# Kernel optimization log

Measured on AMD Instinct MI355X. Metric: run time of the kernel, lower is better.

Reference implementation:

```python
import jax, jax.numpy as jnp
import numpy as np

STRIDE = 8
RATIOS = (0.33, 0.5, 1.0, 2.0, 3.0)
SCALES = (8,)
SEARCH = 255
SCORE = 25                      # (255-127)//8 + 1 + 8
A = len(RATIOS) * len(SCALES)   # 5 anchors per location
THR_HIGH = 0.6
THR_LOW = 0.3
POS_NUM = 16
TOTAL_NUM = 64


def _gen_anchors():
    # Replicates pysot Anchors.generate_all_anchors (corner format, flattened y,x,a)
    base = np.zeros((A, 4), dtype=np.float32)
    sz = STRIDE * STRIDE
    c = 0
    for r in RATIOS:
        ws = int(np.sqrt(sz / r)); hs = int(ws * r)
        for s in SCALES:
            w = ws * s; h = hs * s
            base[c] = [-w * 0.5, -h * 0.5, w * 0.5, h * 0.5]
            c += 1
    ori = SEARCH // 2 - (SCORE // 2) * STRIDE
    xs = ori + STRIDE * np.arange(SCORE, dtype=np.float32)
    cx, cy = np.meshgrid(xs, xs)  # row index = y, col index = x
    ctr = np.stack([cx, cy, cx, cy], -1).reshape(SCORE, SCORE, 1, 4)
    return (base.reshape(1, 1, A, 4) + ctr).reshape(-1, 4).astype(np.float32)


def setup_inputs() -> dict:
    key = jax.random.key(0)
    b, G = 128, 64
    k1, k2 = jax.random.split(key)
    xy = jax.random.uniform(k1, (b, G, 2), minval=0.0, maxval=170.0)
    wh = jax.random.uniform(k2, (b, G, 2), minval=20.0, maxval=70.0)
    gt_boxes = jnp.concatenate([xy, xy + wh], axis=-1)  # valid corner boxes in-image
    return {"gt_boxes": gt_boxes, "anchors": jnp.asarray(_gen_anchors()), "size": SCORE, "neg": 0}


def _overlaps(anchors, gt):
    aw = anchors[:, 2] - anchors[:, 0] + 1.0
    ah = anchors[:, 3] - anchors[:, 1] + 1.0
    area_a = (aw * ah)[None, :, None]
    gw = gt[..., 2] - gt[..., 0] + 1.0
    gh = gt[..., 3] - gt[..., 1] + 1.0
    area_g = (gw * gh)[:, None, :]
    ix = (jnp.minimum(anchors[None, :, None, 2], gt[:, None, :, 2])
          - jnp.maximum(anchors[None, :, None, 0], gt[:, None, :, 0]) + 1.0)
    iy = (jnp.minimum(anchors[None, :, None, 3], gt[:, None, :, 3])
          - jnp.maximum(anchors[None, :, None, 1], gt[:, None, :, 1]) + 1.0)
    inter = jnp.clip(ix, 0.0) * jnp.clip(iy, 0.0)
    return inter / (area_a + area_g - inter)


def _transform(anchors, gt):
    # anchors (N,4), gt (b,N,4) -> (b,N,4) deltas (dx,dy,dw,dh)
    aw = anchors[:, 2] - anchors[:, 0] + 1.0
    ah = anchors[:, 3] - anchors[:, 1] + 1.0
    acx = anchors[:, 0] + 0.5 * aw
    acy = anchors[:, 1] + 0.5 * ah
    gw = gt[..., 2] - gt[..., 0] + 1.0
    gh = gt[..., 3] - gt[..., 1] + 1.0
    gcx = gt[..., 0] + 0.5 * gw
    gcy = gt[..., 1] + 0.5 * gh
    dx = (gcx - acx[None]) / aw[None]
    dy = (gcy - acy[None]) / ah[None]
    dw = jnp.log(gw / aw[None])
    dh = jnp.log(gh / ah[None])
    return jnp.stack([dx, dy, dw, dh], axis=-1)


def reference(gt_boxes, anchors, size, neg):
    b = gt_boxes.shape[0]
    N = anchors.shape[0]
    ov = _overlaps(anchors, gt_boxes)          # (b,N,G) dominant intermediate
    max_ov = jnp.max(ov, axis=2)               # (b,N)
    arg = jnp.argmax(ov, axis=2)               # (b,N)
    gt_max = jnp.max(ov, axis=1)               # (b,G)

    cls = jnp.full((b, N), -1, dtype=jnp.int32)
    cls = jnp.where(max_ov >= THR_HIGH, 1, cls)
    cls = jnp.where(max_ov <= THR_LOW, 0, cls)
    gt_max = jnp.where(gt_max == 0.0, 1e-5, gt_max)
    keep = jnp.sum((ov == gt_max[:, None, :]).astype(jnp.int32), axis=2)
    cls = jnp.where(keep > 0, 1, cls)

    # Deterministic pos/neg subsampling (original uses np.random permutation;
    # we keep the first POS_NUM / TOTAL_NUM by anchor index per batch).
    pos = cls == 1
    cls = jnp.where(pos & (jnp.cumsum(pos.astype(jnp.int32), axis=1) > POS_NUM), -1, cls)
    negm = cls == 0
    cls = jnp.where(negm & (jnp.cumsum(negm.astype(jnp.int32), axis=1) > TOTAL_NUM), -1, cls)

    matched = jnp.take_along_axis(gt_boxes, arg[..., None], axis=1)  # (b,N,4)
    bt = _transform(anchors, matched)                                # (b,N,4)

    # Replicates original bug: pos_num taken from LAST batch element only.
    pos_num = jnp.sum((cls[-1] == 1).astype(jnp.int32))
    bw = jnp.where(cls == 1, 1.0 / pos_num.astype(gt_boxes.dtype), 0.0).astype(gt_boxes.dtype)

    # allowed_border is large -> all anchors inside -> _unmap is identity.
    cls_o = cls.reshape(b, size, size, A).transpose(0, 3, 1, 2)
    bt_o = bt.reshape(b, size, size, A, 4).transpose(0, 4, 3, 1, 2)
    bw_o = bw.reshape(b, size, size, A).transpose(0, 3, 1, 2)
    return cls_o, bt_o, bw_o, max_ov
```

## Files before the change

kernel.cpp:

```cpp
#include <hip/hip_runtime.h>


namespace {
constexpr int B_   = 128;
constexpr int N_   = 3125;
constexpr int G_   = 64;
constexpr int A_   = 5;
constexpr int S_   = 25;
constexpr int POSN = 16;
constexpr int TOTN = 64;

constexpr int CLS_OFF = 0;
constexpr int BT_OFF  = B_ * A_ * S_ * S_;
constexpr int BW_OFF  = BT_OFF + B_ * 4 * A_ * S_ * S_;
constexpr int MO_OFF  = BW_OFF + B_ * A_ * S_ * S_;
}

__device__ __forceinline__ float area_f(float x0, float y0, float x1, float y1) {
#pragma clang fp contract(off)
  return ((x1 - x0) + 1.0f) * ((y1 - y0) + 1.0f);
}

__device__ __forceinline__ float iou_f(float a0, float a1, float a2, float a3,
                                       float aarea, float g0, float g1,
                                       float g2, float g3, float garea) {
#pragma clang fp contract(off)
  float ix = (fminf(a2, g2) - fmaxf(a0, g0)) + 1.0f;
  float iy = (fminf(a3, g3) - fmaxf(a1, g1)) + 1.0f;
  ix = fmaxf(ix, 0.0f);
  iy = fmaxf(iy, 0.0f);
  float inter = ix * iy;
  return inter / ((aarea + garea) - inter);
}

__global__ __launch_bounds__(256) void k1_gtmax(
    const float* __restrict__ gt,
    const float* __restrict__ anchors,
    float* __restrict__ gtmax,
    int* __restrict__ poscnt) {
#pragma clang fp contract(off)
  if (blockIdx.x == 0 && threadIdx.x == 0) poscnt[0] = 0;

  const int t    = threadIdx.x;
  const int lane = t & 63;
  const int w    = blockIdx.x * 4 + (t >> 6);
  const int p0   = w * 2;
  const int b    = p0 >> 6;
  const int g0   = p0 & 63;

  const float4 gg0 = ((const float4*)gt)[b * G_ + g0];
  const float4 gg1 = ((const float4*)gt)[b * G_ + g0 + 1];
  const float ga0 = area_f(gg0.x, gg0.y, gg0.z, gg0.w);
  const float ga1 = area_f(gg1.x, gg1.y, gg1.z, gg1.w);

  float m0 = 0.0f, m1 = 0.0f;
#pragma unroll 4
  for (int i = 0; i < 48; ++i) {
    const int n = i * 64 + lane;
    const float4 aa = ((const float4*)anchors)[n];
    const float aarea = area_f(aa.x, aa.y, aa.z, aa.w);
    m0 = fmaxf(m0, iou_f(aa.x, aa.y, aa.z, aa.w, aarea,
                         gg0.x, gg0.y, gg0.z, gg0.w, ga0));
    m1 = fmaxf(m1, iou_f(aa.x, aa.y, aa.z, aa.w, aarea,
                         gg1.x, gg1.y, gg1.z, gg1.w, ga1));
  }
  {
    const int n = 48 * 64 + lane;
    if (n < N_) {
      const float4 aa = ((const float4*)anchors)[n];
      const float aarea = area_f(aa.x, aa.y, aa.z, aa.w);
      m0 = fmaxf(m0, iou_f(aa.x, aa.y, aa.z, aa.w, aarea,
                           gg0.x, gg0.y, gg0.z, gg0.w, ga0));
      m1 = fmaxf(m1, iou_f(aa.x, aa.y, aa.z, aa.w, aarea,
                           gg1.x, gg1.y, gg1.z, gg1.w, ga1));
    }
  }
#pragma unroll
  for (int off = 32; off > 0; off >>= 1) {
    m0 = fmaxf(m0, __shfl_xor(m0, off, 64));
    m1 = fmaxf(m1, __shfl_xor(m1, off, 64));
  }
  if (lane == 0) {
    gtmax[p0]     = m0;
    gtmax[p0 + 1] = m1;
  }
}

__global__ __launch_bounds__(256) void k2_anchor(
    const float* __restrict__ gt, const float* __restrict__ anchors,
    const float* __restrict__ gtmax, float* __restrict__ out,
    int* __restrict__ cls0, int* __restrict__ poscnt) {
#pragma clang fp contract(off)
  const int b = blockIdx.y;
  const int t = threadIdx.x;
  const int n = blockIdx.x * 256 + t;

  __shared__ float s_gt[G_ * 4];
  __shared__ float s_garea[G_];
  __shared__ float s_gtmax[G_];
  __shared__ int   s_pc;

  if (t == 0) s_pc = 0;
  s_gt[t] = gt[b * G_ * 4 + t];
  __syncthreads();
  if (t < G_) {
    s_garea[t] =
        area_f(s_gt[t * 4 + 0], s_gt[t * 4 + 1], s_gt[t * 4 + 2], s_gt[t * 4 + 3]);
    const float v = gtmax[b * G_ + t];
    s_gtmax[t] = (v == 0.0f) ? 1e-5f : v;
  }
  __syncthreads();

  if (n < N_) {
    const float4 aa = ((const float4*)anchors)[n];
    const float aw = (aa.z - aa.x) + 1.0f;
    const float ah = (aa.w - aa.y) + 1.0f;
    const float aarea = aw * ah;

    float best = -1.0f;
    int barg = 0;
    int keep = 0;
#pragma unroll 8
    for (int g = 0; g < G_; ++g) {
      const float4 gg = *(const float4*)&s_gt[g * 4];
      const float v = iou_f(aa.x, aa.y, aa.z, aa.w, aarea,
                            gg.x, gg.y, gg.z, gg.w, s_garea[g]);
      if (v > best) { best = v; barg = g; }
      keep |= (v == s_gtmax[g]);
    }

    int cc = -1;
    if (best >= 0.6f) cc = 1;
    if (best <= 0.3f) cc = 0;
    if (keep) cc = 1;
    cls0[b * N_ + n] = cc;
    if (b == B_ - 1 && cc == 1) atomicAdd(&s_pc, 1);

    const float m0 = s_gt[barg * 4 + 0], m1 = s_gt[barg * 4 + 1];
    const float m2 = s_gt[barg * 4 + 2], m3 = s_gt[barg * 4 + 3];
    const float gw = (m2 - m0) + 1.0f;
    const float gh = (m3 - m1) + 1.0f;
    const float acx = aa.x + 0.5f * aw;
    const float acy = aa.y + 0.5f * ah;
    const float gcx = m0 + 0.5f * gw;
    const float gcy = m1 + 0.5f * gh;
    const float dx = (gcx - acx) / aw;
    const float dy = (gcy - acy) / ah;
    const float dw = logf(gw / aw);
    const float dh = logf(gh / ah);

    const int a = n % A_;
    const int rem = n / A_;
    const int x = rem % S_;
    const int y = rem / S_;
    const int spat = y * S_ + x;

    float* __restrict__ out_bt = out + BT_OFF;
    const int btb = ((b * 4 + 0) * A_ + a) * (S_ * S_) + spat;
    out_bt[btb + 0 * A_ * S_ * S_] = dx;
    out_bt[btb + 1 * A_ * S_ * S_] = dy;
    out_bt[btb + 2 * A_ * S_ * S_] = dw;
    out_bt[btb + 3 * A_ * S_ * S_] = dh;

    out[MO_OFF + b * N_ + n] = best;
  }
  __syncthreads();
  if (t == 0 && b == B_ - 1 && s_pc > 0) atomicAdd(poscnt, s_pc);
}

__global__ __launch_bounds__(256) void k3_caps_bw(
    float* __restrict__ out, const int* __restrict__ cls0,
    const int* __restrict__ poscnt) {
  const int b = blockIdx.x;
  const int t = threadIdx.x;
  __shared__ int s_c[N_];
  __shared__ int s_p[256];
  __shared__ int s_n[256];

#pragma unroll
  for (int k = 0; k < 13; ++k) {
    const int i = k * 256 + t;
    if (i < N_) s_c[i] = cls0[b * N_ + i];
  }
  __syncthreads();

  const int n0 = t * 13;
  int cvals[13];
  int myp = 0, myn = 0;
#pragma unroll
  for (int k = 0; k < 13; ++k) {
    const int n = n0 + k;
    int cc = -1;
    if (n < N_) {
      cc = s_c[n];
      if (cc == 1) ++myp;
      else if (cc == 0) ++myn;
    }
    cvals[k] = cc;
  }
  s_p[t] = myp;
  s_n[t] = myn;
  __syncthreads();
  for (int off = 1; off < 256; off <<= 1) {
    int vp = 0, vn = 0;
    if (t >= off) { vp = s_p[t - off]; vn = s_n[t - off]; }
    __syncthreads();
    s_p[t] += vp;
    s_n[t] += vn;
    __syncthreads();
  }

  int runp = s_p[t] - myp;
  int runn = s_n[t] - myn;
#pragma unroll
  for (int k = 0; k < 13; ++k) {
    const int n = n0 + k;
    if (n >= N_) break;
    int cc = cvals[k];
    if (cc == 1) {
      if (++runp > POSN) cc = -1;
    } else if (cc == 0) {
      if (++runn > TOTN) cc = -1;
    }
    s_c[n] = __float_as_int((float)cc);
  }
  __syncthreads();

  const int pc = poscnt[0];
  const float inv = 1.0f / (float)((pc < POSN) ? pc : POSN);

#pragma unroll
  for (int k = 0; k < 13; ++k) {
    const int o = k * 256 + t;
    if (o < N_) {
      const int a  = o / 625;
      const int sp = o % 625;
      const float v = __int_as_float(s_c[sp * 5 + a]);
      out[CLS_OFF + b * N_ + o] = v;
      out[BW_OFF + b * N_ + o] = (v == 1.0f) ? inv : 0.0f;
    }
  }
}

extern "C" void kernel_launch(void* const* d_in, const int* in_sizes, int n_in,
                              void* d_out, int out_size, void* d_ws,
                              size_t ws_size, hipStream_t stream) {
  const float* gt = (const float*)d_in[0];
  const float* anchors = (const float*)d_in[1];
  float* out = (float*)d_out;
  int* poscnt = (int*)d_ws;
  float* gtmax = (float*)d_ws + 64;
  int* cls0 = (int*)d_ws + 64 + B_ * G_;

  k1_gtmax<<<1024, 256, 0, stream>>>(gt, anchors, gtmax, poscnt);
  k2_anchor<<<dim3(13, B_), 256, 0, stream>>>(gt, anchors, gtmax, out, cls0,
                                              poscnt);
  k3_caps_bw<<<B_, 256, 0, stream>>>(out, cls0, poscnt);
}
```

Before: 113.7 us.

## Separable gt-max IoU via per-axis overlap and fuse cap kernel into anchor kernel

The gt-max kernel no longer scans all 3125 anchors. It uses the regular anchor grid: for each anchor shape it takes the maximum x-overlap and y-overlap across grid positions with wave shuffles and multiplies them, with anchor sizes and areas hard-coded as constants. The third kernel is folded into the second using a per-batch ticket counter, so the last block of each batch does the pos/neg capping. Blocks then spin until the last batch finishes before writing box weights. This removes one launch and most of the gt-max arithmetic, but it depends on the fixed anchor geometry and adds a cross-block spin wait that could stall or deadlock if blocks are not co-resident.

```diff
diff --git a/kernel.cpp b/kernel.cpp
--- a/kernel.cpp
+++ b/kernel.cpp
@@ -35,61 +35,53 @@
 
 __global__ __launch_bounds__(256) void k1_gtmax(
     const float* __restrict__ gt,
-    const float* __restrict__ anchors,
     float* __restrict__ gtmax,
-    int* __restrict__ poscnt) {
-#pragma clang fp contract(off)
-  if (blockIdx.x == 0 && threadIdx.x == 0) poscnt[0] = 0;
-
-  const int t    = threadIdx.x;
+    int* __restrict__ arr) {
+#pragma clang fp contract(off)
+  const int t = threadIdx.x;
+  if (blockIdx.x == 0 && t < 1 + B_) arr[t] = 0;
+
   const int lane = t & 63;
-  const int w    = blockIdx.x * 4 + (t >> 6);
-  const int p0   = w * 2;
-  const int b    = p0 >> 6;
-  const int g0   = p0 & 63;
-
-  const float4 gg0 = ((const float4*)gt)[b * G_ + g0];
-  const float4 gg1 = ((const float4*)gt)[b * G_ + g0 + 1];
-  const float ga0 = area_f(gg0.x, gg0.y, gg0.z, gg0.w);
-  const float ga1 = area_f(gg1.x, gg1.y, gg1.z, gg1.w);
-
-  float m0 = 0.0f, m1 = 0.0f;
-#pragma unroll 4
-  for (int i = 0; i < 48; ++i) {
-    const int n = i * 64 + lane;
-    const float4 aa = ((const float4*)anchors)[n];
-    const float aarea = area_f(aa.x, aa.y, aa.z, aa.w);
-    m0 = fmaxf(m0, iou_f(aa.x, aa.y, aa.z, aa.w, aarea,
-                         gg0.x, gg0.y, gg0.z, gg0.w, ga0));
-    m1 = fmaxf(m1, iou_f(aa.x, aa.y, aa.z, aa.w, aarea,
-                         gg1.x, gg1.y, gg1.z, gg1.w, ga1));
-  }
-  {
-    const int n = 48 * 64 + lane;
-    if (n < N_) {
-      const float4 aa = ((const float4*)anchors)[n];
-      const float aarea = area_f(aa.x, aa.y, aa.z, aa.w);
-      m0 = fmaxf(m0, iou_f(aa.x, aa.y, aa.z, aa.w, aarea,
-                           gg0.x, gg0.y, gg0.z, gg0.w, ga0));
-      m1 = fmaxf(m1, iou_f(aa.x, aa.y, aa.z, aa.w, aarea,
-                           gg1.x, gg1.y, gg1.z, gg1.w, ga1));
-    }
-  }
-#pragma unroll
-  for (int off = 32; off > 0; off >>= 1) {
-    m0 = fmaxf(m0, __shfl_xor(m0, off, 64));
-    m1 = fmaxf(m1, __shfl_xor(m1, off, 64));
-  }
-  if (lane == 0) {
-    gtmax[p0]     = m0;
-    gtmax[p0 + 1] = m1;
-  }
-}
-
-__global__ __launch_bounds__(256) void k2_anchor(
+  const int pair = blockIdx.x * 4 + (t >> 6);
+  const int b = pair >> 6;
+  const int g = pair & 63;
+
+  const float4 gg = ((const float4*)gt)[b * G_ + g];
+  const float garea = area_f(gg.x, gg.y, gg.z, gg.w);
+
+  const int half = lane >> 5;
+  const int p = lane & 31;
+  const float c = 31.0f + 8.0f * (float)p;
+  const float Glo = half ? gg.y : gg.x;
+  const float Ghi = half ? gg.w : gg.z;
+  const bool valid = p < S_;
+
+  const float HW[A_] = {52.f, 44.f, 32.f, 20.f, 16.f};
+  const float HH[A_] = {16.f, 20.f, 32.f, 40.f, 48.f};
+  const float AA[A_] = {3465.f, 3649.f, 4225.f, 3321.f, 3201.f};
+
+  float m = 0.0f;
+#pragma unroll
+  for (int s = 0; s < A_; ++s) {
+    const float H = half ? HH[s] : HW[s];
+    float v = (fminf(c + H, Ghi) - fmaxf(c - H, Glo)) + 1.0f;
+    v = fmaxf(v, 0.0f);
+    if (!valid) v = 0.0f;
+#pragma unroll
+    for (int off = 1; off < 32; off <<= 1)
+      v = fmaxf(v, __shfl_xor(v, off, 64));
+    const float other = __shfl_xor(v, 32, 64);
+    const float inter = v * other;
+    const float uni = (AA[s] + garea) - inter;
+    m = fmaxf(m, inter / uni);
+  }
+  if (lane == 0) gtmax[pair] = m;
+}
+
+__global__ __launch_bounds__(256) void k2_fused(
     const float* __restrict__ gt, const float* __restrict__ anchors,
     const float* __restrict__ gtmax, float* __restrict__ out,
-    int* __restrict__ cls0, int* __restrict__ poscnt) {
+    int* __restrict__ cls0, int* __restrict__ arr) {
 #pragma clang fp contract(off)
   const int b = blockIdx.y;
   const int t = threadIdx.x;
@@ -99,6 +91,11 @@
   __shared__ float s_garea[G_];
   __shared__ float s_gtmax[G_];
   __shared__ int   s_pc;
+  __shared__ int   s_ticket;
+  __shared__ float s_inv;
+  __shared__ int   s_c[N_];
+  __shared__ int   s_p[256];
+  __shared__ int   s_n[256];
 
   if (t == 0) s_pc = 0;
   s_gt[t] = gt[b * G_ * 4 + t];
@@ -133,7 +130,8 @@
     if (best >= 0.6f) cc = 1;
     if (best <= 0.3f) cc = 0;
     if (keep) cc = 1;
-    cls0[b * N_ + n] = cc;
+    __hip_atomic_store(&cls0[b * N_ + n], cc, __ATOMIC_RELAXED,
+                       __HIP_MEMORY_SCOPE_AGENT);
     if (b == B_ - 1 && cc == 1) atomicAdd(&s_pc, 1);
 
     const float m0 = s_gt[barg * 4 + 0], m1 = s_gt[barg * 4 + 1];
@@ -165,38 +163,35 @@
     out[MO_OFF + b * N_ + n] = best;
   }
   __syncthreads();
-  if (t == 0 && b == B_ - 1 && s_pc > 0) atomicAdd(poscnt, s_pc);
-}
-
-__global__ __launch_bounds__(256) void k3_caps_bw(
-    float* __restrict__ out, const int* __restrict__ cls0,
-    const int* __restrict__ poscnt) {
-  const int b = blockIdx.x;
-  const int t = threadIdx.x;
-  __shared__ int s_c[N_];
-  __shared__ int s_p[256];
-  __shared__ int s_n[256];
-
+
+  if (t == 0) {
+    if (b == B_ - 1 && s_pc > 0) atomicAdd(&arr[0], s_pc);
+    __threadfence();
+    s_ticket = atomicAdd(&arr[1 + b], 1);
+  }
+  __syncthreads();
+  if (s_ticket != 12) return;
+
+  __threadfence();
 #pragma unroll
   for (int k = 0; k < 13; ++k) {
     const int i = k * 256 + t;
-    if (i < N_) s_c[i] = cls0[b * N_ + i];
+    if (i < N_)
+      s_c[i] = __hip_atomic_load(&cls0[b * N_ + i], __ATOMIC_RELAXED,
+                                 __HIP_MEMORY_SCOPE_AGENT);
   }
   __syncthreads();
 
   const int n0 = t * 13;
-  int cvals[13];
   int myp = 0, myn = 0;
 #pragma unroll
   for (int k = 0; k < 13; ++k) {
-    const int n = n0 + k;
-    int cc = -1;
-    if (n < N_) {
-      cc = s_c[n];
-      if (cc == 1) ++myp;
-      else if (cc == 0) ++myn;
-    }
-    cvals[k] = cc;
+    const int nn = n0 + k;
+    if (nn < N_) {
+      const int cc = s_c[nn];
+      myp += (cc == 1);
+      myn += (cc == 0);
+    }
   }
   s_p[t] = myp;
   s_n[t] = myn;
@@ -214,20 +209,41 @@
   int runn = s_n[t] - myn;
 #pragma unroll
   for (int k = 0; k < 13; ++k) {
-    const int n = n0 + k;
-    if (n >= N_) break;
-    int cc = cvals[k];
+    const int nn = n0 + k;
+    if (nn >= N_) break;
+    int cc = s_c[nn];
     if (cc == 1) {
       if (++runp > POSN) cc = -1;
     } else if (cc == 0) {
       if (++runn > TOTN) cc = -1;
     }
-    s_c[n] = __float_as_int((float)cc);
-  }
-  __syncthreads();
-
-  const int pc = poscnt[0];
-  const float inv = 1.0f / (float)((pc < POSN) ? pc : POSN);
+    s_c[nn] = __float_as_int((float)cc);
+  }
+  __syncthreads();
+
+#pragma unroll
+  for (int k = 0; k < 13; ++k) {
+    const int o = k * 256 + t;
+    if (o < N_) {
+      const int a  = o / 625;
+      const int sp = o % 625;
+      out[CLS_OFF + b * N_ + o] = __int_as_float(s_c[sp * 5 + a]);
+    }
+  }
+
+  if (t == 0) {
+    if (b != B_ - 1) {
+      int guard = 0;
+      while (atomicAdd(&arr[1 + (B_ - 1)], 0) < 13 && guard < 200000) {
+        __builtin_amdgcn_s_sleep(8);
+        ++guard;
+      }
+    }
+    __threadfence();
+    const int pc = atomicAdd(&arr[0], 0);
+    s_inv = 1.0f / (float)((pc < POSN) ? pc : POSN);
+  }
+  __syncthreads();
 
 #pragma unroll
   for (int k = 0; k < 13; ++k) {
@@ -236,8 +252,7 @@
       const int a  = o / 625;
       const int sp = o % 625;
       const float v = __int_as_float(s_c[sp * 5 + a]);
-      out[CLS_OFF + b * N_ + o] = v;
-      out[BW_OFF + b * N_ + o] = (v == 1.0f) ? inv : 0.0f;
+      out[BW_OFF + b * N_ + o] = (v == 1.0f) ? s_inv : 0.0f;
     }
   }
 }
@@ -248,12 +263,11 @@
   const float* gt = (const float*)d_in[0];
   const float* anchors = (const float*)d_in[1];
   float* out = (float*)d_out;
-  int* poscnt = (int*)d_ws;
-  float* gtmax = (float*)d_ws + 64;
-  int* cls0 = (int*)d_ws + 64 + B_ * G_;
-
-  k1_gtmax<<<1024, 256, 0, stream>>>(gt, anchors, gtmax, poscnt);
-  k2_anchor<<<dim3(13, B_), 256, 0, stream>>>(gt, anchors, gtmax, out, cls0,
-                                              poscnt);
-  k3_caps_bw<<<B_, 256, 0, stream>>>(out, cls0, poscnt);
-}
+  int* arr = (int*)d_ws;
+  float* gtmax = (float*)d_ws + 256;
+  int* cls0 = (int*)d_ws + 256 + B_ * G_;
+
+  k1_gtmax<<<2048, 256, 0, stream>>>(gt, gtmax, arr);
+  k2_fused<<<dim3(13, B_), 256, 0, stream>>>(gt, anchors, gtmax, out, cls0,
+                                             arr);
+}
```

Measured after the change: 174.0 us. 1.53x slower.

## Compute per-gt max IoU separably from anchor grid, drop gtmax kernel

Applied to the files above, without the earlier changes.

Removes the first kernel, which brute-forced IoU over all 3125 anchors per gt box. Because the anchors form a regular grid, each block now computes the per-gt maximum IoU from per-axis maximum overlaps using hardcoded anchor half-sizes and areas. The atomic positive counter is replaced by per-block partial counts that the last kernel sums. This saves a launch and a full IoU sweep, but hardcodes anchor geometry taken from the test's anchor generator. Taking the max of each axis overlap separately assumes the IoU peak is where both overlaps peak together, which may not match the reference exactly.

```diff
diff --git a/kernel.cpp b/kernel.cpp
--- a/kernel.cpp
+++ b/kernel.cpp
@@ -33,63 +33,12 @@
   return inter / ((aarea + garea) - inter);
 }
 
-__global__ __launch_bounds__(256) void k1_gtmax(
+__global__ __launch_bounds__(256) void k2_main(
     const float* __restrict__ gt,
     const float* __restrict__ anchors,
-    float* __restrict__ gtmax,
-    int* __restrict__ poscnt) {
-#pragma clang fp contract(off)
-  if (blockIdx.x == 0 && threadIdx.x == 0) poscnt[0] = 0;
-
-  const int t    = threadIdx.x;
-  const int lane = t & 63;
-  const int w    = blockIdx.x * 4 + (t >> 6);
-  const int p0   = w * 2;
-  const int b    = p0 >> 6;
-  const int g0   = p0 & 63;
-
-  const float4 gg0 = ((const float4*)gt)[b * G_ + g0];
-  const float4 gg1 = ((const float4*)gt)[b * G_ + g0 + 1];
-  const float ga0 = area_f(gg0.x, gg0.y, gg0.z, gg0.w);
-  const float ga1 = area_f(gg1.x, gg1.y, gg1.z, gg1.w);
-
-  float m0 = 0.0f, m1 = 0.0f;
-#pragma unroll 4
-  for (int i = 0; i < 48; ++i) {
-    const int n = i * 64 + lane;
-    const float4 aa = ((const float4*)anchors)[n];
-    const float aarea = area_f(aa.x, aa.y, aa.z, aa.w);
-    m0 = fmaxf(m0, iou_f(aa.x, aa.y, aa.z, aa.w, aarea,
-                         gg0.x, gg0.y, gg0.z, gg0.w, ga0));
-    m1 = fmaxf(m1, iou_f(aa.x, aa.y, aa.z, aa.w, aarea,
-                         gg1.x, gg1.y, gg1.z, gg1.w, ga1));
-  }
-  {
-    const int n = 48 * 64 + lane;
-    if (n < N_) {
-      const float4 aa = ((const float4*)anchors)[n];
-      const float aarea = area_f(aa.x, aa.y, aa.z, aa.w);
-      m0 = fmaxf(m0, iou_f(aa.x, aa.y, aa.z, aa.w, aarea,
-                           gg0.x, gg0.y, gg0.z, gg0.w, ga0));
-      m1 = fmaxf(m1, iou_f(aa.x, aa.y, aa.z, aa.w, aarea,
-                           gg1.x, gg1.y, gg1.z, gg1.w, ga1));
-    }
-  }
-#pragma unroll
-  for (int off = 32; off > 0; off >>= 1) {
-    m0 = fmaxf(m0, __shfl_xor(m0, off, 64));
-    m1 = fmaxf(m1, __shfl_xor(m1, off, 64));
-  }
-  if (lane == 0) {
-    gtmax[p0]     = m0;
-    gtmax[p0 + 1] = m1;
-  }
-}
-
-__global__ __launch_bounds__(256) void k2_anchor(
-    const float* __restrict__ gt, const float* __restrict__ anchors,
-    const float* __restrict__ gtmax, float* __restrict__ out,
-    int* __restrict__ cls0, int* __restrict__ poscnt) {
+    float* __restrict__ out,
+    int* __restrict__ cls0,
+    int* __restrict__ pos_part) {
 #pragma clang fp contract(off)
   const int b = blockIdx.y;
   const int t = threadIdx.x;
@@ -98,16 +47,50 @@
   __shared__ float s_gt[G_ * 4];
   __shared__ float s_garea[G_];
   __shared__ float s_gtmax[G_];
+  __shared__ float s_ax[G_][2][A_];
   __shared__ int   s_pc;
 
   if (t == 0) s_pc = 0;
   s_gt[t] = gt[b * G_ * 4 + t];
   __syncthreads();
+
+  if (t < 2 * G_) {
+    const int g    = t >> 1;
+    const int axis = t & 1;
+    const float Glo = s_gt[g * 4 + axis];
+    const float Ghi = s_gt[g * 4 + 2 + axis];
+#pragma unroll
+    for (int s = 0; s < A_; ++s) {
+      const float HW[A_] = {52.f, 44.f, 32.f, 20.f, 16.f};
+      const float HH[A_] = {16.f, 20.f, 32.f, 40.f, 48.f};
+      const float H = axis ? HH[s] : HW[s];
+      float mx = 0.0f;
+#pragma unroll
+      for (int p = 0; p < S_; ++p) {
+        const float c = 31.0f + 8.0f * (float)p;
+        float v = (fminf(c + H, Ghi) - fmaxf(c - H, Glo)) + 1.0f;
+        mx = fmaxf(mx, fmaxf(v, 0.0f));
+      }
+      s_ax[g][axis][s] = mx;
+    }
+  }
   if (t < G_) {
     s_garea[t] =
         area_f(s_gt[t * 4 + 0], s_gt[t * 4 + 1], s_gt[t * 4 + 2], s_gt[t * 4 + 3]);
-    const float v = gtmax[b * G_ + t];
-    s_gtmax[t] = (v == 0.0f) ? 1e-5f : v;
+  }
+  __syncthreads();
+
+  if (t < G_) {
+    const float AA[A_] = {3465.f, 3649.f, 4225.f, 3321.f, 3201.f};
+    const float garea = s_garea[t];
+    float m = 0.0f;
+#pragma unroll
+    for (int s = 0; s < A_; ++s) {
+      const float inter = s_ax[t][0][s] * s_ax[t][1][s];
+      const float uni = (AA[s] + garea) - inter;
+      m = fmaxf(m, inter / uni);
+    }
+    s_gtmax[t] = (m == 0.0f) ? 1e-5f : m;
   }
   __syncthreads();
 
@@ -165,18 +148,20 @@
     out[MO_OFF + b * N_ + n] = best;
   }
   __syncthreads();
-  if (t == 0 && b == B_ - 1 && s_pc > 0) atomicAdd(poscnt, s_pc);
+  if (t == 0 && b == B_ - 1) pos_part[blockIdx.x] = s_pc;
 }
 
 __global__ __launch_bounds__(256) void k3_caps_bw(
     float* __restrict__ out, const int* __restrict__ cls0,
-    const int* __restrict__ poscnt) {
+    const int* __restrict__ pos_part) {
   const int b = blockIdx.x;
   const int t = threadIdx.x;
   __shared__ int s_c[N_];
   __shared__ int s_p[256];
   __shared__ int s_n[256];
-
+  __shared__ int s_parts[16];
+
+  if (t < 13) s_parts[t] = pos_part[t];
 #pragma unroll
   for (int k = 0; k < 13; ++k) {
     const int i = k * 256 + t;
@@ -226,7 +211,9 @@
   }
   __syncthreads();
 
-  const int pc = poscnt[0];
+  int pc = 0;
+#pragma unroll
+  for (int k = 0; k < 13; ++k) pc += s_parts[k];
   const float inv = 1.0f / (float)((pc < POSN) ? pc : POSN);
 
 #pragma unroll
@@ -248,12 +235,9 @@
   const float* gt = (const float*)d_in[0];
   const float* anchors = (const float*)d_in[1];
   float* out = (float*)d_out;
-  int* poscnt = (int*)d_ws;
-  float* gtmax = (float*)d_ws + 64;
-  int* cls0 = (int*)d_ws + 64 + B_ * G_;
-
-  k1_gtmax<<<1024, 256, 0, stream>>>(gt, anchors, gtmax, poscnt);
-  k2_anchor<<<dim3(13, B_), 256, 0, stream>>>(gt, anchors, gtmax, out, cls0,
-                                              poscnt);
-  k3_caps_bw<<<B_, 256, 0, stream>>>(out, cls0, poscnt);
-}
+  int* pos_part = (int*)d_ws;
+  int* cls0 = (int*)d_ws + 64;
+
+  k2_main<<<dim3(13, B_), 256, 0, stream>>>(gt, anchors, out, cls0, pos_part);
+  k3_caps_bw<<<B_, 256, 0, stream>>>(out, cls0, pos_part);
+}
```

Result: faster. 96.21 us (-15.4%).
